# Performance work log

Measured on AMD Instinct MI355X. Metric: run time of the kernel, lower is better.

Reference implementation:

```python
import jax, jax.numpy as jnp
import numpy as np

N_NODES = 100000
N_EDGES = 1200000
N_GRAPHS = 256
IN_DIM = 15
HID = 64


def setup_inputs() -> dict:
    key = jax.random.key(0)
    ks = jax.random.split(key, 12)
    x = jax.random.normal(ks[0], (N_NODES, IN_DIM), dtype=jnp.float32)
    edge_index = jax.random.randint(ks[1], (2, N_EDGES), 0, N_NODES, dtype=jnp.int64)
    batch = jnp.sort(jax.random.randint(ks[2], (N_NODES,), 0, N_GRAPHS, dtype=jnp.int64))
    def glorot(k, fan_in, fan_out):
        lim = jnp.sqrt(6.0 / (fan_in + fan_out)).astype(jnp.float32)
        return jax.random.uniform(k, (fan_in, fan_out), jnp.float32, -lim, lim)
    return {
        'x': x, 'edge_index': edge_index, 'batch': batch,
        'W1': glorot(ks[3], IN_DIM, HID), 'b1': jnp.zeros((HID,), jnp.float32),
        'W2': glorot(ks[4], HID, HID),    'b2': jnp.zeros((HID,), jnp.float32),
        'W3': glorot(ks[5], HID, HID),    'b3': jnp.zeros((HID,), jnp.float32),
        'W4': glorot(ks[6], HID, HID),    'b4': jnp.zeros((HID,), jnp.float32),
    }


def _gcn_conv(x, src, dst, norm, W, b):
    # GCNConv: h = x @ W; out[dst] += norm * h[src]; out += b
    h = x @ W                      # [N, out]
    msg = h[src] * norm[:, None]   # [E+N, out] gather + scale
    out = jax.ops.segment_sum(msg, dst, num_segments=N_NODES)
    return out + b


def reference(x, edge_index, batch, W1, b1, W2, b2, W3, b3, W4, b4):
    # gcn_norm with self-loops (PyG default): A_hat = D^-1/2 (A+I) D^-1/2
    loop = jnp.arange(N_NODES, dtype=edge_index.dtype)
    src = jnp.concatenate([edge_index[0], loop])
    dst = jnp.concatenate([edge_index[1], loop])
    deg = jax.ops.segment_sum(jnp.ones_like(src, dtype=x.dtype), dst, num_segments=N_NODES)
    dinv = jnp.where(deg > 0, jax.lax.rsqrt(deg), 0.0)
    norm = dinv[src] * dinv[dst]   # [E+N]

    h = jax.nn.relu(_gcn_conv(x, src, dst, norm, W1, b1))
    h = jax.nn.relu(_gcn_conv(h, src, dst, norm, W2, b2))
    h = jax.nn.relu(_gcn_conv(h, src, dst, norm, W3, b3))
    h = jax.nn.relu(_gcn_conv(h, src, dst, norm, W4, b4))

    # global_mean_pool over batch ids
    sums = jax.ops.segment_sum(h, batch, num_segments=N_GRAPHS)
    cnt = jax.ops.segment_sum(jnp.ones((N_NODES,), h.dtype), batch, num_segments=N_GRAPHS)
    return sums / jnp.maximum(cnt, 1.0)[:, None]
```

## Files before the change

### kernel.cpp

```cpp
#include <hip/hip_runtime.h>
#include <hip/hip_bf16.h>

#define NN 100000
#define NE 1200000
#define NG 256
#define NB 256
#define BSZ 391
#define NBK1 128
#define ECH 9376
#define MAXB 6144
#define NBND_BLK 391
#define NPAD_BLK 6250

typedef __attribute__((ext_vector_type(8))) short bf16x8;
typedef __attribute__((ext_vector_type(4))) float f32x4;

__device__ __forceinline__ unsigned f2b(float f) {
    unsigned b = __float_as_uint(f);
    return (b + 0x7FFFu + ((b >> 16) & 1u)) >> 16;
}
__device__ __forceinline__ float b2f(unsigned short u) {
    return __uint_as_float((unsigned)u << 16);
}
__device__ __forceinline__ float4 b2f4(ushort4 u) {
    return make_float4(b2f(u.x), b2f(u.y), b2f(u.z), b2f(u.w));
}
__device__ __forceinline__ void add_u4(float* a, uint4 v) {
    const unsigned* u = (const unsigned*)&v;
#pragma unroll
    for (int i = 0; i < 4; ++i) {
        a[2*i]   += __uint_as_float(u[i] << 16);
        a[2*i+1] += __uint_as_float(u[i] & 0xFFFF0000u);
    }
}

__global__ void ph0_hist(const int* __restrict__ dst, int* __restrict__ hrows) {
    __shared__ int h[NB];
    const int t = threadIdx.x;
    h[t] = 0;
    __syncthreads();
    const int e0 = blockIdx.x * ECH;
    const int cnt = min(ECH, NE - e0);
    for (int i = t; i < cnt; i += 256)
        atomicAdd(&h[dst[e0 + i] / BSZ], 1);
    __syncthreads();
    hrows[blockIdx.x * NB + t] = h[t];
}

__global__ void ph_scanA(const int* __restrict__ hrows, int* __restrict__ chunkoff,
                         int* __restrict__ btot) {
    __shared__ int s[NBK1];
    const int b = threadIdx.x;
    const int t = blockIdx.x;
    int v = hrows[b * NB + t];
    s[b] = v;
    __syncthreads();
    for (int off = 1; off < NBK1; off <<= 1) {
        int u = (b >= off) ? s[b - off] : 0;
        __syncthreads();
        s[b] += u;
        __syncthreads();
    }
    chunkoff[b * NB + t] = s[b] - v;
    if (b == NBK1 - 1) btot[t] = s[b];
}

__global__ void ph_scanB(const int* __restrict__ btot, int* __restrict__ bbase,
                         int* __restrict__ row_off) {
    __shared__ int s[NB];
    const int t = threadIdx.x;
    int v = btot[t];
    s[t] = v;
    __syncthreads();
    for (int off = 1; off < NB; off <<= 1) {
        int u = (t >= off) ? s[t - off] : 0;
        __syncthreads();
        s[t] += u;
        __syncthreads();
    }
    bbase[t] = s[t] - v;
    if (t == NB - 1) { bbase[NB] = NE; row_off[NN] = NE; }
}

__global__ void ph1_bucketize(const int* __restrict__ src, const int* __restrict__ dst,
                              const int* __restrict__ chunkoff, const int* __restrict__ bbase,
                              unsigned* __restrict__ barray) {
    __shared__ int lbase[NB];
    __shared__ int lcur[NB];
    const int t = threadIdx.x;
    lbase[t] = bbase[t] + chunkoff[blockIdx.x * NB + t];
    lcur[t] = 0;
    __syncthreads();
    const int e0 = blockIdx.x * ECH;
    const int cnt = min(ECH, NE - e0);
    for (int i = t; i < cnt; i += 256) {
        int d = dst[e0 + i], s = src[e0 + i];
        int b = d / BSZ;
        int pos = lbase[b] + atomicAdd(&lcur[b], 1);
        barray[pos] = ((unsigned)(d - b * BSZ) << 17) | (unsigned)s;
    }
}

__global__ void ph2_build(const unsigned* __restrict__ barray, const int* __restrict__ bbase,
                          int* __restrict__ row_off, float* __restrict__ dinv,
                          int* __restrict__ csr) {
    __shared__ unsigned estage[MAXB];
    __shared__ int lcsr[MAXB];
    __shared__ int s[512];
    __shared__ int cur[BSZ];
    const int t = threadIdx.x;
    const int b = blockIdx.x;
    const int ebase = bbase[b];
    const int cnt = bbase[b + 1] - ebase;
    const int nbase = b * BSZ;
    const int nnodes = min(BSZ, NN - nbase);
    s[t] = 0; s[t + 256] = 0;
    __syncthreads();
    for (int i = t; i < cnt; i += 256) {
        unsigned e = barray[ebase + i];
        estage[i] = e;
        atomicAdd(&s[e >> 17], 1);
    }
    __syncthreads();
    for (int off = 1; off < 512; off <<= 1) {
        int v1 = (t >= off) ? s[t - off] : 0;
        int v2 = s[t + 256 - off];
        __syncthreads();
        s[t] += v1; s[t + 256] += v2;
        __syncthreads();
    }
    for (int l = t; l < nnodes; l += 256) {
        int incl = s[l];
        int excl = l ? s[l - 1] : 0;
        row_off[nbase + l] = ebase + excl;
        dinv[nbase + l] = rsqrtf((float)(incl - excl) + 1.0f);
        cur[l] = excl;
    }
    __syncthreads();
    for (int i = t; i < cnt; i += 256) {
        unsigned e = estage[i];
        int pos = atomicAdd(&cur[e >> 17], 1);
        lcsr[pos] = (int)(e & 0x1FFFFu);
    }
    __syncthreads();
    for (int i = t; i < cnt; i += 256)
        csr[ebase + i] = lcsr[i];
}

__global__ void k_prep(const float* __restrict__ W2, const float* __restrict__ W3,
                       const float* __restrict__ W4, unsigned short* __restrict__ wt,
                       const float* __restrict__ x, const float* __restrict__ dinv,
                       unsigned short* __restrict__ xs,
                       const int* __restrict__ batch, int* __restrict__ gstart) {
    const int blk = blockIdx.x;
    const int t = threadIdx.x;
    if (blk < 3) {
        const float* W = (blk == 0) ? W2 : (blk == 1) ? W3 : W4;
        unsigned short* o = wt + blk * 8192;
        const int n = t >> 2;
        const int j0 = (t & 3) * 16;
#pragma unroll
        for (int j = 0; j < 16; ++j) {
            float wv = W[(j0 + j) * 64 + n];
            unsigned short h = (unsigned short)f2b(wv);
            o[n * 64 + j0 + j] = h;
            o[4096 + n * 64 + j0 + j] = (unsigned short)f2b(wv - b2f(h));
        }
    } else if (blk < 3 + NBND_BLK) {
        int i = (blk - 3) * 256 + t;
        if (i >= NN) return;
        int b = batch[i];
        if (i == 0) {
            for (int g = 0; g <= b; ++g) gstart[g] = 0;
        } else {
            int bp = batch[i - 1];
            for (int g = bp + 1; g <= b; ++g) gstart[g] = i;
        }
        if (i == NN - 1) {
            for (int g = b + 1; g <= NG; ++g) gstart[g] = NN;
        }
    } else {
        int i = (blk - 3 - NBND_BLK) * 256 + t;
        if (i < NN * 16) {
            int n = i >> 4, k = i & 15;
            float v = (k < 15) ? dinv[n] * x[n * 15 + k] : 0.f;
            xs[i] = (unsigned short)f2b(v);
        }
    }
}

__global__ void fused1(const unsigned short* __restrict__ xs, const int* __restrict__ row_off,
                       const int* __restrict__ csr, const float* __restrict__ dinv,
                       const float* __restrict__ W, const float* __restrict__ bias,
                       unsigned* __restrict__ out) {
    __shared__ float4 Wl[16][16];
    __shared__ float  al[64][20];
    const int t = threadIdx.x;
    if (t < 240) Wl[t >> 4][t & 15] = ((const float4*)W)[t];
    if (t < 16) Wl[15][t] = make_float4(0,0,0,0);
    const int nl = t >> 2, c4 = t & 3;
    const int node = blockIdx.x * 64 + nl;
    float4 acc = make_float4(0,0,0,0);
    float dv = 0.f;
    if (node < NN) {
        const ushort4* base = (const ushort4*)xs;
        acc = b2f4(base[(size_t)node * 4 + c4]);
        int p = row_off[node], e = row_off[node + 1];
        for (; p + 3 < e; p += 4) {
            int s0 = csr[p], s1 = csr[p+1], s2 = csr[p+2], s3 = csr[p+3];
            float4 a = b2f4(base[(size_t)s0 * 4 + c4]);
            float4 b = b2f4(base[(size_t)s1 * 4 + c4]);
            float4 c = b2f4(base[(size_t)s2 * 4 + c4]);
            float4 d = b2f4(base[(size_t)s3 * 4 + c4]);
            acc.x += (a.x + b.x) + (c.x + d.x);
            acc.y += (a.y + b.y) + (c.y + d.y);
            acc.z += (a.z + b.z) + (c.z + d.z);
            acc.w += (a.w + b.w) + (c.w + d.w);
        }
        for (; p < e; ++p) {
            float4 a = b2f4(base[(size_t)csr[p] * 4 + c4]);
            acc.x += a.x; acc.y += a.y; acc.z += a.z; acc.w += a.w;
        }
        dv = dinv[node];
        acc.x *= dv; acc.y *= dv; acc.z *= dv; acc.w *= dv;
    }
    ((float4*)&al[nl][0])[c4] = acc;
    __syncthreads();
    if (node >= NN) return;
    float4 o0 = ((const float4*)bias)[c4 * 4 + 0];
    float4 o1 = ((const float4*)bias)[c4 * 4 + 1];
    float4 o2 = ((const float4*)bias)[c4 * 4 + 2];
    float4 o3 = ((const float4*)bias)[c4 * 4 + 3];
#pragma unroll
    for (int k = 0; k < 16; ++k) {
        float a = al[nl][k];
        float4 w0 = Wl[k][c4 * 4 + 0];
        float4 w1 = Wl[k][c4 * 4 + 1];
        float4 w2 = Wl[k][c4 * 4 + 2];
        float4 w3 = Wl[k][c4 * 4 + 3];
        o0.x = fmaf(a, w0.x, o0.x); o0.y = fmaf(a, w0.y, o0.y); o0.z = fmaf(a, w0.z, o0.z); o0.w = fmaf(a, w0.w, o0.w);
        o1.x = fmaf(a, w1.x, o1.x); o1.y = fmaf(a, w1.y, o1.y); o1.z = fmaf(a, w1.z, o1.z); o1.w = fmaf(a, w1.w, o1.w);
        o2.x = fmaf(a, w2.x, o2.x); o2.y = fmaf(a, w2.y, o2.y); o2.z = fmaf(a, w2.z, o2.z); o2.w = fmaf(a, w2.w, o2.w);
        o3.x = fmaf(a, w3.x, o3.x); o3.y = fmaf(a, w3.y, o3.y); o3.z = fmaf(a, w3.z, o3.z); o3.w = fmaf(a, w3.w, o3.w);
    }
    float dv2 = dv;
    o0.x = fmaxf(o0.x, 0.f) * dv2; o0.y = fmaxf(o0.y, 0.f) * dv2; o0.z = fmaxf(o0.z, 0.f) * dv2; o0.w = fmaxf(o0.w, 0.f) * dv2;
    o1.x = fmaxf(o1.x, 0.f) * dv2; o1.y = fmaxf(o1.y, 0.f) * dv2; o1.z = fmaxf(o1.z, 0.f) * dv2; o1.w = fmaxf(o1.w, 0.f) * dv2;
    o2.x = fmaxf(o2.x, 0.f) * dv2; o2.y = fmaxf(o2.y, 0.f) * dv2; o2.z = fmaxf(o2.z, 0.f) * dv2; o2.w = fmaxf(o2.w, 0.f) * dv2;
    o3.x = fmaxf(o3.x, 0.f) * dv2; o3.y = fmaxf(o3.y, 0.f) * dv2; o3.z = fmaxf(o3.z, 0.f) * dv2; o3.w = fmaxf(o3.w, 0.f) * dv2;
    uint4 lo, hi;
    lo.x = f2b(o0.x) | (f2b(o0.y) << 16);
    lo.y = f2b(o0.z) | (f2b(o0.w) << 16);
    lo.z = f2b(o1.x) | (f2b(o1.y) << 16);
    lo.w = f2b(o1.z) | (f2b(o1.w) << 16);
    hi.x = f2b(o2.x) | (f2b(o2.y) << 16);
    hi.y = f2b(o2.z) | (f2b(o2.w) << 16);
    hi.z = f2b(o3.x) | (f2b(o3.y) << 16);
    hi.w = f2b(o3.z) | (f2b(o3.w) << 16);
    uint4* ob = (uint4*)out + (size_t)node * 8 + c4 * 2;
    ob[0] = lo; ob[1] = hi;
}

template <bool LAST>
__global__ __launch_bounds__(256) void fused64(const unsigned short* __restrict__ g,
                        const int* __restrict__ row_off, const int* __restrict__ csr,
                        const float* __restrict__ dinv, const unsigned short* __restrict__ wt,
                        const float* __restrict__ bias, void* __restrict__ outv) {
    __shared__ alignas(16) unsigned short Ahi[16][72];
    __shared__ alignas(16) unsigned short Alo[16][72];
    __shared__ alignas(16) unsigned short Bhi[64][72];
    __shared__ alignas(16) unsigned short Blo[64][72];
    __shared__ alignas(16) float dinv_l[16];
    const int t = threadIdx.x;

    {
        const uint4* srcv = (const uint4*)wt;
#pragma unroll
        for (int i = 0; i < 4; ++i) {
            int idx = t + i * 256;
            uint4 v = srcv[idx];
            int sel = idx >> 9, r = idx & 511;
            int n = r >> 3, kc = r & 7;
            unsigned short* dstp = sel ? &Blo[n][kc * 8] : &Bhi[n][kc * 8];
            *(uint4*)dstp = v;
        }
    }

    const int nl = t >> 4;
    const int s8 = (t >> 3) & 1;
    const int q  = t & 7;
    const int node = blockIdx.x * 16 + nl;
    float acc[8] = {0,0,0,0,0,0,0,0};
    const float dv = dinv[node];
    {
        const uint4* fbase = (const uint4*)g;
        const int r0 = row_off[node], r1 = row_off[node + 1];
        const int half = (r1 - r0 + 1) >> 1;
        int p = r0 + s8 * half;
        const int e = s8 ? r1 : (r0 + half);
        if (s8 == 0) add_u4(acc, fbase[(size_t)node * 8 + q]);
        int i0 = csr[p],   i1 = csr[p+1], i2 = csr[p+2], i3 = csr[p+3];
        int i4 = csr[p+4], i5 = csr[p+5], i6 = csr[p+6], i7 = csr[p+7];
        while (p < e) {
            const int rem = e - p;
            uint4 v0, v1, v2, v3, v4, v5, v6, v7;
            v0 = fbase[(size_t)i0 * 8 + q];
            if (rem > 1) v1 = fbase[(size_t)i1 * 8 + q];
            if (rem > 2) v2 = fbase[(size_t)i2 * 8 + q];
            if (rem > 3) v3 = fbase[(size_t)i3 * 8 + q];
            if (rem > 4) v4 = fbase[(size_t)i4 * 8 + q];
            if (rem > 5) v5 = fbase[(size_t)i5 * 8 + q];
            if (rem > 6) v6 = fbase[(size_t)i6 * 8 + q];
            if (rem > 7) v7 = fbase[(size_t)i7 * 8 + q];
            p += 8;
            i0 = csr[p];   i1 = csr[p+1]; i2 = csr[p+2]; i3 = csr[p+3];
            i4 = csr[p+4]; i5 = csr[p+5]; i6 = csr[p+6]; i7 = csr[p+7];
            add_u4(acc, v0);
            if (rem > 1) add_u4(acc, v1);
            if (rem > 2) add_u4(acc, v2);
            if (rem > 3) add_u4(acc, v3);
            if (rem > 4) add_u4(acc, v4);
            if (rem > 5) add_u4(acc, v5);
            if (rem > 6) add_u4(acc, v6);
            if (rem > 7) add_u4(acc, v7);
        }
    }
#pragma unroll
    for (int i = 0; i < 8; ++i) acc[i] += __shfl_xor(acc[i], 8, 64);
    if (s8 == 0) {
        uint4 uh, ul;
        unsigned* uhp = (unsigned*)&uh;
        unsigned* ulp = (unsigned*)&ul;
#pragma unroll
        for (int i = 0; i < 4; ++i) {
            float va = acc[2*i] * dv;
            float vb = acc[2*i+1] * dv;
            unsigned ha = f2b(va), hb = f2b(vb);
            unsigned la = f2b(va - b2f((unsigned short)ha));
            unsigned lb = f2b(vb - b2f((unsigned short)hb));
            uhp[i] = ha | (hb << 16);
            ulp[i] = la | (lb << 16);
        }
        *(uint4*)&Ahi[nl][q * 8] = uh;
        *(uint4*)&Alo[nl][q * 8] = ul;
        if (q == 0) dinv_l[nl] = dv;
    }
    __syncthreads();

    const int wid = t >> 6;
    const int l = t & 63;
    const int rr = l & 15;
    const int kb = l >> 4;
    f32x4 c = {0.f, 0.f, 0.f, 0.f};
#pragma unroll
    for (int ks = 0; ks < 2; ++ks) {
        bf16x8 ah = *(const bf16x8*)&Ahi[rr][ks * 32 + kb * 8];
        bf16x8 am = *(const bf16x8*)&Alo[rr][ks * 32 + kb * 8];
        bf16x8 bh = *(const bf16x8*)&Bhi[wid * 16 + rr][ks * 32 + kb * 8];
        bf16x8 bl = *(const bf16x8*)&Blo[wid * 16 + rr][ks * 32 + kb * 8];
        c = __builtin_amdgcn_mfma_f32_16x16x32_bf16(ah, bh, c, 0, 0, 0);
        c = __builtin_amdgcn_mfma_f32_16x16x32_bf16(ah, bl, c, 0, 0, 0);
        c = __builtin_amdgcn_mfma_f32_16x16x32_bf16(am, bh, c, 0, 0, 0);
    }
    float bv = bias[wid * 16 + rr];
    float4 dq = *(const float4*)&dinv_l[kb * 4];
    const float* dqp = (const float*)&dq;
#pragma unroll
    for (int r = 0; r < 4; ++r) {
        int nd = blockIdx.x * 16 + kb * 4 + r;
        float o = fmaxf(c[r] + bv, 0.f);
        if (!LAST) {
            o *= dqp[r];
            ((unsigned short*)outv)[(size_t)nd * 64 + wid * 16 + rr] = (unsigned short)f2b(o);
        } else {
            ((float*)outv)[(size_t)nd * 64 + wid * 16 + rr] = o;
        }
    }
}

__global__ void k_pool(const float* __restrict__ h, const int* __restrict__ gstart,
                       float* __restrict__ out) {
    __shared__ float s[4][64];
    int g = blockIdx.x;
    int t = threadIdx.x, lane = t & 63, w = t >> 6;
    int r0 = gstart[g], r1 = gstart[g + 1];
    float acc = 0.f;
    for (int r = r0 + w; r < r1; r += 4) acc += h[(size_t)r * 64 + lane];
    s[w][lane] = acc;
    __syncthreads();
    if (t < 64) {
        float v = s[0][t] + s[1][t] + s[2][t] + s[3][t];
        float c = (float)(r1 - r0);
        out[g * 64 + t] = v / fmaxf(c, 1.f);
    }
}

static inline size_t al256(size_t x) { return (x + 255) & ~(size_t)255; }

extern "C" void kernel_launch(void* const* d_in, const int* in_sizes, int n_in,
                              void* d_out, int out_size, void* d_ws, size_t ws_size,
                              hipStream_t stream) {
    const float* x     = (const float*)d_in[0];
    const int*   eidx  = (const int*)d_in[1];
    const int*   batch = (const int*)d_in[2];
    const float* W1 = (const float*)d_in[3];  const float* b1 = (const float*)d_in[4];
    const float* W2 = (const float*)d_in[5];  const float* b2 = (const float*)d_in[6];
    const float* W3 = (const float*)d_in[7];  const float* b3 = (const float*)d_in[8];
    const float* W4 = (const float*)d_in[9];  const float* b4 = (const float*)d_in[10];
    float* out = (float*)d_out;
    (void)in_sizes; (void)n_in; (void)out_size; (void)ws_size;

    const int* src = eidx;
    const int* dst = eidx + NE;

    char* p = (char*)d_ws;
    size_t off = 0;
    int*   hrows   = (int*)(p + off);   off = al256(off + sizeof(int) * NBK1 * NB);
    int*   chunkoff= (int*)(p + off);   off = al256(off + sizeof(int) * NBK1 * NB);
    int*   btot    = (int*)(p + off);   off = al256(off + sizeof(int) * NB);
    int*   bbase   = (int*)(p + off);   off = al256(off + sizeof(int) * (NB + 1));
    int*   gstart  = (int*)(p + off);   off = al256(off + sizeof(int) * (NG + 1));
    int*   row_off = (int*)(p + off);   off = al256(off + sizeof(int) * (NN + 1));
    float* dinv    = (float*)(p + off); off = al256(off + sizeof(float) * NN);
    unsigned short* wt = (unsigned short*)(p + off); off = al256(off + sizeof(short) * 3 * 8192);
    int*   csr     = (int*)(p + off);   off = al256(off + sizeof(int) * (NE + 16));
    unsigned short* F0 = (unsigned short*)(p + off); off = al256(off + sizeof(short) * (size_t)NN * 64);
    unsigned short* F1 = (unsigned short*)(p + off); off = al256(off + sizeof(short) * (size_t)NN * 64);
    float* H4      = (float*)(p + off); off = al256(off + sizeof(float) * (size_t)NN * 64);
    unsigned*       barray = (unsigned*)H4;
    unsigned short* xs     = F1;

    ph0_hist     <<<NBK1, 256, 0, stream>>>(dst, hrows);
    ph_scanA     <<<NB, NBK1, 0, stream>>>(hrows, chunkoff, btot);
    ph_scanB     <<<1, NB, 0, stream>>>(btot, bbase, row_off);
    ph1_bucketize<<<NBK1, 256, 0, stream>>>(src, dst, chunkoff, bbase, barray);
    ph2_build    <<<NB, 256, 0, stream>>>(barray, bbase, row_off, dinv, csr);
    k_prep       <<<3 + NBND_BLK + NPAD_BLK, 256, 0, stream>>>(W2, W3, W4, wt, x, dinv, xs, batch, gstart);

    fused1        <<<(NN + 63) / 64, 256, 0, stream>>>(xs, row_off, csr, dinv, W1, b1, (unsigned*)F0);
    fused64<false><<<NN / 16, 256, 0, stream>>>(F0, row_off, csr, dinv, wt,        b2, F1);
    fused64<false><<<NN / 16, 256, 0, stream>>>(F1, row_off, csr, dinv, wt + 8192, b3, F0);
    fused64<true> <<<NN / 16, 256, 0, stream>>>(F0, row_off, csr, dinv, wt + 16384,b4, H4);

    k_pool  <<<NG, 256, 0, stream>>>(H4, gstart, out);
}
```

Baseline: 180.7 us.

## Split feature dims into slabs, separating gather-aggregation from MFMA matmul

```diff
diff --git a/kernel.cpp b/kernel.cpp
--- a/kernel.cpp
+++ b/kernel.cpp
@@ -11,6 +11,7 @@
 #define MAXB 6144
 #define NBND_BLK 391
 #define NPAD_BLK 6250
+#define ACH 1563
 
 typedef __attribute__((ext_vector_type(8))) short bf16x8;
 typedef __attribute__((ext_vector_type(4))) float f32x4;
@@ -192,7 +193,7 @@
 __global__ void fused1(const unsigned short* __restrict__ xs, const int* __restrict__ row_off,
                        const int* __restrict__ csr, const float* __restrict__ dinv,
                        const float* __restrict__ W, const float* __restrict__ bias,
-                       unsigned* __restrict__ out) {
+                       unsigned short* __restrict__ outG) {
     __shared__ float4 Wl[16][16];
     __shared__ float  al[64][20];
     const int t = threadIdx.x;
@@ -257,22 +258,73 @@
     hi.y = f2b(o2.z) | (f2b(o2.w) << 16);
     hi.z = f2b(o3.x) | (f2b(o3.y) << 16);
     hi.w = f2b(o3.z) | (f2b(o3.w) << 16);
-    uint4* ob = (uint4*)out + (size_t)node * 8 + c4 * 2;
-    ob[0] = lo; ob[1] = hi;
+    uint4* ob = (uint4*)(outG + (size_t)c4 * NN * 16);
+    ob[(size_t)node * 2] = lo;
+    ob[(size_t)node * 2 + 1] = hi;
+}
+
+__global__ void agg_slice(const unsigned short* __restrict__ G, const int* __restrict__ row_off,
+                          const int* __restrict__ csr, const float* __restrict__ dinv,
+                          unsigned short* __restrict__ A) {
+    const int bid = blockIdx.x;
+    const int s = bid & 3;
+    const int chunk = bid >> 2;
+    const int t = threadIdx.x;
+    const int nl = t >> 2;
+    const int ll = t & 3;
+    const int node = chunk * 64 + nl;
+    if (node >= NN) return;
+    const uint4* slab = (const uint4*)(G + (size_t)s * NN * 16);
+    float acc[16];
+#pragma unroll
+    for (int j = 0; j < 16; ++j) acc[j] = 0.f;
+    const int r0 = row_off[node], r1 = row_off[node + 1];
+    if (ll == 0) {
+        add_u4(acc,     slab[(size_t)node * 2]);
+        add_u4(acc + 8, slab[(size_t)node * 2 + 1]);
+    }
+    int p = r0 + ll;
+    int i0 = csr[p], i1 = csr[p + 4], i2 = csr[p + 8], i3 = csr[p + 12];
+    while (p < r1) {
+        const int rem = r1 - p;
+        uint4 a0, b0, a1, b1, a2, b2, a3, b3;
+        a0 = slab[(size_t)i0 * 2]; b0 = slab[(size_t)i0 * 2 + 1];
+        if (rem > 4)  { a1 = slab[(size_t)i1 * 2]; b1 = slab[(size_t)i1 * 2 + 1]; }
+        if (rem > 8)  { a2 = slab[(size_t)i2 * 2]; b2 = slab[(size_t)i2 * 2 + 1]; }
+        if (rem > 12) { a3 = slab[(size_t)i3 * 2]; b3 = slab[(size_t)i3 * 2 + 1]; }
+        p += 16;
+        i0 = csr[p]; i1 = csr[p + 4]; i2 = csr[p + 8]; i3 = csr[p + 12];
+        add_u4(acc, a0); add_u4(acc + 8, b0);
+        if (rem > 4)  { add_u4(acc, a1); add_u4(acc + 8, b1); }
+        if (rem > 8)  { add_u4(acc, a2); add_u4(acc + 8, b2); }
+        if (rem > 12) { add_u4(acc, a3); add_u4(acc + 8, b3); }
+    }
+#pragma unroll
+    for (int j = 0; j < 16; ++j) acc[j] += __shfl_xor(acc[j], 1, 64);
+#pragma unroll
+    for (int j = 0; j < 16; ++j) acc[j] += __shfl_xor(acc[j], 2, 64);
+    const float dv = dinv[node];
+    float q0 = acc[0], q1 = acc[1], q2 = acc[2], q3 = acc[3];
+    if (ll == 1) { q0 = acc[4];  q1 = acc[5];  q2 = acc[6];  q3 = acc[7];  }
+    if (ll == 2) { q0 = acc[8];  q1 = acc[9];  q2 = acc[10]; q3 = acc[11]; }
+    if (ll == 3) { q0 = acc[12]; q1 = acc[13]; q2 = acc[14]; q3 = acc[15]; }
+    q0 *= dv; q1 *= dv; q2 *= dv; q3 *= dv;
+    uint2 u;
+    u.x = f2b(q0) | (f2b(q1) << 16);
+    u.y = f2b(q2) | (f2b(q3) << 16);
+    *(uint2*)(A + (size_t)s * NN * 16 + (size_t)node * 16 + ll * 4) = u;
 }
 
 template <bool LAST>
-__global__ __launch_bounds__(256) void fused64(const unsigned short* __restrict__ g,
-                        const int* __restrict__ row_off, const int* __restrict__ csr,
+__global__ __launch_bounds__(256) void mm_slice(const unsigned short* __restrict__ A,
                         const float* __restrict__ dinv, const unsigned short* __restrict__ wt,
                         const float* __restrict__ bias, void* __restrict__ outv) {
-    __shared__ alignas(16) unsigned short Ahi[16][72];
-    __shared__ alignas(16) unsigned short Alo[16][72];
+    __shared__ alignas(16) unsigned short Al[16][72];
     __shared__ alignas(16) unsigned short Bhi[64][72];
     __shared__ alignas(16) unsigned short Blo[64][72];
     __shared__ alignas(16) float dinv_l[16];
     const int t = threadIdx.x;
-
+    const int n0 = blockIdx.x * 16;
     {
         const uint4* srcv = (const uint4*)wt;
 #pragma unroll
@@ -285,68 +337,15 @@
             *(uint4*)dstp = v;
         }
     }
-
-    const int nl = t >> 4;
-    const int s8 = (t >> 3) & 1;
-    const int q  = t & 7;
-    const int node = blockIdx.x * 16 + nl;
-    float acc[8] = {0,0,0,0,0,0,0,0};
-    const float dv = dinv[node];
-    {
-        const uint4* fbase = (const uint4*)g;
-        const int r0 = row_off[node], r1 = row_off[node + 1];
-        const int half = (r1 - r0 + 1) >> 1;
-        int p = r0 + s8 * half;
-        const int e = s8 ? r1 : (r0 + half);
-        if (s8 == 0) add_u4(acc, fbase[(size_t)node * 8 + q]);
-        int i0 = csr[p],   i1 = csr[p+1], i2 = csr[p+2], i3 = csr[p+3];
-        int i4 = csr[p+4], i5 = csr[p+5], i6 = csr[p+6], i7 = csr[p+7];
-        while (p < e) {
-            const int rem = e - p;
-            uint4 v0, v1, v2, v3, v4, v5, v6, v7;
-            v0 = fbase[(size_t)i0 * 8 + q];
-            if (rem > 1) v1 = fbase[(size_t)i1 * 8 + q];
-            if (rem > 2) v2 = fbase[(size_t)i2 * 8 + q];
-            if (rem > 3) v3 = fbase[(size_t)i3 * 8 + q];
-            if (rem > 4) v4 = fbase[(size_t)i4 * 8 + q];
-            if (rem > 5) v5 = fbase[(size_t)i5 * 8 + q];
-            if (rem > 6) v6 = fbase[(size_t)i6 * 8 + q];
-            if (rem > 7) v7 = fbase[(size_t)i7 * 8 + q];
-            p += 8;
-            i0 = csr[p];   i1 = csr[p+1]; i2 = csr[p+2]; i3 = csr[p+3];
-            i4 = csr[p+4]; i5 = csr[p+5]; i6 = csr[p+6]; i7 = csr[p+7];
-            add_u4(acc, v0);
-            if (rem > 1) add_u4(acc, v1);
-            if (rem > 2) add_u4(acc, v2);
-            if (rem > 3) add_u4(acc, v3);
-            if (rem > 4) add_u4(acc, v4);
-            if (rem > 5) add_u4(acc, v5);
-            if (rem > 6) add_u4(acc, v6);
-            if (rem > 7) add_u4(acc, v7);
-        }
-    }
-#pragma unroll
-    for (int i = 0; i < 8; ++i) acc[i] += __shfl_xor(acc[i], 8, 64);
-    if (s8 == 0) {
-        uint4 uh, ul;
-        unsigned* uhp = (unsigned*)&uh;
-        unsigned* ulp = (unsigned*)&ul;
-#pragma unroll
-        for (int i = 0; i < 4; ++i) {
-            float va = acc[2*i] * dv;
-            float vb = acc[2*i+1] * dv;
-            unsigned ha = f2b(va), hb = f2b(vb);
-            unsigned la = f2b(va - b2f((unsigned short)ha));
-            unsigned lb = f2b(vb - b2f((unsigned short)hb));
-            uhp[i] = ha | (hb << 16);
-            ulp[i] = la | (lb << 16);
-        }
-        *(uint4*)&Ahi[nl][q * 8] = uh;
-        *(uint4*)&Alo[nl][q * 8] = ul;
-        if (q == 0) dinv_l[nl] = dv;
-    }
-    __syncthreads();
-
+    if (t < 128) {
+        int s = t >> 5, r = t & 31;
+        int nloc = r >> 1, half = r & 1;
+        uint4 v = ((const uint4*)A)[(size_t)s * NN * 2 + (size_t)(n0 + nloc) * 2 + half];
+        *(uint4*)&Al[nloc][s * 16 + half * 8] = v;
+    } else if (t < 144) {
+        dinv_l[t - 128] = dinv[n0 + t - 128];
+    }
+    __syncthreads();
     const int wid = t >> 6;
     const int l = t & 63;
     const int rr = l & 15;
@@ -354,24 +353,22 @@
     f32x4 c = {0.f, 0.f, 0.f, 0.f};
 #pragma unroll
     for (int ks = 0; ks < 2; ++ks) {
-        bf16x8 ah = *(const bf16x8*)&Ahi[rr][ks * 32 + kb * 8];
-        bf16x8 am = *(const bf16x8*)&Alo[rr][ks * 32 + kb * 8];
+        bf16x8 a  = *(const bf16x8*)&Al[rr][ks * 32 + kb * 8];
         bf16x8 bh = *(const bf16x8*)&Bhi[wid * 16 + rr][ks * 32 + kb * 8];
         bf16x8 bl = *(const bf16x8*)&Blo[wid * 16 + rr][ks * 32 + kb * 8];
-        c = __builtin_amdgcn_mfma_f32_16x16x32_bf16(ah, bh, c, 0, 0, 0);
-        c = __builtin_amdgcn_mfma_f32_16x16x32_bf16(ah, bl, c, 0, 0, 0);
-        c = __builtin_amdgcn_mfma_f32_16x16x32_bf16(am, bh, c, 0, 0, 0);
+        c = __builtin_amdgcn_mfma_f32_16x16x32_bf16(a, bh, c, 0, 0, 0);
+        c = __builtin_amdgcn_mfma_f32_16x16x32_bf16(a, bl, c, 0, 0, 0);
     }
     float bv = bias[wid * 16 + rr];
     float4 dq = *(const float4*)&dinv_l[kb * 4];
     const float* dqp = (const float*)&dq;
 #pragma unroll
     for (int r = 0; r < 4; ++r) {
-        int nd = blockIdx.x * 16 + kb * 4 + r;
+        int nd = n0 + kb * 4 + r;
         float o = fmaxf(c[r] + bv, 0.f);
         if (!LAST) {
             o *= dqp[r];
-            ((unsigned short*)outv)[(size_t)nd * 64 + wid * 16 + rr] = (unsigned short)f2b(o);
+            ((unsigned short*)outv)[(size_t)wid * NN * 16 + (size_t)nd * 16 + rr] = (unsigned short)f2b(o);
         } else {
             ((float*)outv)[(size_t)nd * 64 + wid * 16 + rr] = o;
         }
@@ -424,11 +421,12 @@
     float* dinv    = (float*)(p + off); off = al256(off + sizeof(float) * NN);
     unsigned short* wt = (unsigned short*)(p + off); off = al256(off + sizeof(short) * 3 * 8192);
     int*   csr     = (int*)(p + off);   off = al256(off + sizeof(int) * (NE + 16));
-    unsigned short* F0 = (unsigned short*)(p + off); off = al256(off + sizeof(short) * (size_t)NN * 64);
-    unsigned short* F1 = (unsigned short*)(p + off); off = al256(off + sizeof(short) * (size_t)NN * 64);
+    unsigned short* F0   = (unsigned short*)(p + off); off = al256(off + sizeof(short) * (size_t)NN * 64);
+    unsigned short* F1   = (unsigned short*)(p + off); off = al256(off + sizeof(short) * (size_t)NN * 64);
+    unsigned short* Abuf = (unsigned short*)(p + off); off = al256(off + sizeof(short) * (size_t)NN * 64);
     float* H4      = (float*)(p + off); off = al256(off + sizeof(float) * (size_t)NN * 64);
     unsigned*       barray = (unsigned*)H4;
-    unsigned short* xs     = F1;
+    unsigned short* xs     = Abuf;
 
     ph0_hist     <<<NBK1, 256, 0, stream>>>(dst, hrows);
     ph_scanA     <<<NB, NBK1, 0, stream>>>(hrows, chunkoff, btot);
@@ -437,10 +435,13 @@
     ph2_build    <<<NB, 256, 0, stream>>>(barray, bbase, row_off, dinv, csr);
     k_prep       <<<3 + NBND_BLK + NPAD_BLK, 256, 0, stream>>>(W2, W3, W4, wt, x, dinv, xs, batch, gstart);
 
-    fused1        <<<(NN + 63) / 64, 256, 0, stream>>>(xs, row_off, csr, dinv, W1, b1, (unsigned*)F0);
-    fused64<false><<<NN / 16, 256, 0, stream>>>(F0, row_off, csr, dinv, wt,        b2, F1);
-    fused64<false><<<NN / 16, 256, 0, stream>>>(F1, row_off, csr, dinv, wt + 8192, b3, F0);
-    fused64<true> <<<NN / 16, 256, 0, stream>>>(F0, row_off, csr, dinv, wt + 16384,b4, H4);
+    fused1       <<<(NN + 63) / 64, 256, 0, stream>>>(xs, row_off, csr, dinv, W1, b1, F0);
+    agg_slice    <<<ACH * 4, 256, 0, stream>>>(F0, row_off, csr, dinv, Abuf);
+    mm_slice<false><<<NN / 16, 256, 0, stream>>>(Abuf, dinv, wt,         b2, F1);
+    agg_slice    <<<ACH * 4, 256, 0, stream>>>(F1, row_off, csr, dinv, Abuf);
+    mm_slice<false><<<NN / 16, 256, 0, stream>>>(Abuf, dinv, wt + 8192,  b3, F0);
+    agg_slice    <<<ACH * 4, 256, 0, stream>>>(F0, row_off, csr, dinv, Abuf);
+    mm_slice<true> <<<NN / 16, 256, 0, stream>>>(Abuf, dinv, wt + 16384, b4, H4);
 
     k_pool  <<<NG, 256, 0, stream>>>(H4, gstart, out);
 }
```

Result: slower. 365.1 us (+102.0%).
